# Kernel tuning notes

Hardware: AMD Instinct MI355X
Metric: run time of the kernel (lower is better)

Reference implementation:

```python
import jax, jax.numpy as jnp
import numpy as np
from jax import lax

# PSTConv constants (match init_kwargs)
R = 0.5            # ball-query radius
K = 32             # neighbors per anchor
SPATIAL_STRIDE = 2
TK = 3             # temporal kernel size (odd)
TSTRIDE = 1        # temporal stride
PAD = (1, 1)       # temporal padding, 'zeros' mode
MID = 128
OUT = 256


def setup_inputs() -> dict:
    key = jax.random.key(0)
    k1, k2, k3, k4, k5 = jax.random.split(key, 5)
    B, L, N, C = 8, 6, 2048, 64
    xyzs = jax.random.uniform(k1, (B, L, N, 3), dtype=jnp.float32)
    features = jax.random.normal(k2, (B, L, C, N), dtype=jnp.float32)
    # kaiming_uniform with size=[mid, in+3, 1, 1]: bound = 1/sqrt(in_planes+3)
    b = 1.0 / np.sqrt(C + 3)
    w_d = jax.random.uniform(k3, (MID, 3), minval=-b, maxval=b, dtype=jnp.float32)
    w_f = jax.random.uniform(k4, (MID, C), minval=-b, maxval=b, dtype=jnp.float32)
    bt = 1.0 / np.sqrt(TK * MID)
    w_t = jax.random.uniform(k5, (OUT, TK * MID), minval=-bt, maxval=bt, dtype=jnp.float32)
    return {"xyzs": xyzs, "features": features, "w_d": w_d, "w_f": w_f, "w_t": w_t}


def _fps(xyz, m):
    # furthest point sampling on [N,3]; CUDA kernel starts from index 0
    N = xyz.shape[0]
    def step(carry, _):
        dists, far = carry
        d = jnp.sum((xyz - xyz[far]) ** 2, axis=-1)
        dists = jnp.minimum(dists, d)
        nxt = jnp.argmax(dists).astype(jnp.int32)
        return (dists, nxt), far
    init = (jnp.full((N,), 1e10, dtype=xyz.dtype), jnp.int32(0))
    _, idx = lax.scan(step, init, None, length=m)
    return idx  # [m] int32


def _ball_query(nbr_xyz, anchor_xyz):
    # nbr_xyz [B,N,3], anchor_xyz [B,M,3] -> [B,M,K] int32 indices into N
    # Semantics of pointnet2 ball_query: first K points (in index order) within
    # radius R; slots past the count are filled with the first found index
    # (0 if no point is in range).
    N = nbr_xyz.shape[1]
    d2 = jnp.sum((anchor_xyz[:, :, None, :] - nbr_xyz[:, None, :, :]) ** 2, axis=-1)  # [B,M,N]
    vals = jnp.where(d2 < R * R, jnp.arange(N, dtype=jnp.int32), jnp.int32(N))
    neg_top, _ = lax.top_k(-vals, K)          # K smallest indices, ascending
    idx = -neg_top                            # [B,M,K]
    first = idx[..., :1]
    fill = jnp.where(first < N, first, 0)
    return jnp.where(idx < N, idx, fill)


def _group(feat, idx):
    # feat [B,C,N], idx [B,M,K] -> [B,C,M,K]
    return jax.vmap(lambda f, i: f[:, i])(feat, idx)


def reference(xyzs, features, w_d, w_f, w_t):
    B, L, N, _ = xyzs.shape
    M = N // SPATIAL_STRIDE
    rad = TK // 2
    # zero temporal padding
    zx = jnp.zeros((B, 1, N, 3), xyzs.dtype)
    zf = jnp.zeros((B, 1, features.shape[2], N), features.dtype)
    xp = jnp.concatenate([zx] * PAD[0] + [xyzs] + [zx] * PAD[1], axis=1)
    fp = jnp.concatenate([zf] * PAD[0] + [features] + [zf] * PAD[1], axis=1)
    Lp = L + PAD[0] + PAD[1]

    new_xyzs, new_feats = [], []
    fps_b = jax.vmap(lambda x: _fps(x, M))
    for t in range(rad, Lp - rad, TSTRIDE):
        xyz_t = xp[:, t]                                   # [B,N,3]
        aidx = fps_b(xyz_t)                                # [B,M]
        anchor = jnp.take_along_axis(xyz_t, aidx[:, :, None], axis=1)  # [B,M,3]
        anchor_c = jnp.transpose(anchor, (0, 2, 1))[:, :, :, None]     # [B,3,M,1]
        sfs = []
        for i in range(t - rad, t + rad + 1):
            idx = _ball_query(xp[:, i], anchor)            # [B,M,K]
            g_xyz = _group(jnp.transpose(xp[:, i], (0, 2, 1)), idx)    # [B,3,M,K]
            disp = g_xyz - anchor_c
            d = jnp.einsum('oc,bcmk->bomk', w_d, disp)     # [B,MID,M,K]
            g_f = _group(fp[:, i], idx)                    # [B,C,M,K]
            f = jnp.einsum('oc,bcmk->bomk', w_f, g_f)
            sfs.append(jnp.max(f + d, axis=-1))            # [B,MID,M]
        sf = jax.nn.relu(jnp.concatenate(sfs, axis=1))     # [B,TK*MID,M]
        new_feats.append(jnp.einsum('oc,bcm->bom', w_t, sf))
        new_xyzs.append(anchor)
    return jnp.stack(new_xyzs, axis=1), jnp.stack(new_feats, axis=1)
```

## Files before the change

### kernel.cpp

```cpp
#include <hip/hip_runtime.h>

#define BATCH 8
#define LFRM  6
#define NP    2048
#define MP    1024
#define CIN   64
#define MIDC  128
#define OUTC  256
#define TKM   384
#define KNN   32
#define RAD2  0.25f

#define FPS_BLOCKS (BATCH * LFRM)
#define WT_BLOCKS  ((OUTC * TKM) / (256 * 4))
#define FT_BLOCKS  (BATCH * LFRM * (NP / 64))
#define WFS 132

typedef float f2 __attribute__((ext_vector_type(2)));
typedef float f32x4 __attribute__((ext_vector_type(4)));
typedef _Float16 f16x8 __attribute__((ext_vector_type(8)));
typedef _Float16 f16x4 __attribute__((ext_vector_type(4)));

union SharedU {
  struct {
    float4 pts[NP];
    unsigned long long wk[2][4];
  } fps;
  struct {
    float ftile[CIN][64];
    float wfT[CIN][WFS];
    float xt[64], yt[64], zt[64];
    float wdl[MIDC * 3];
  } ft;
};

__device__ __forceinline__ uint64_t kmax64(uint64_t a, uint64_t b) {
  return a > b ? a : b;
}
template <int CTRL>
__device__ __forceinline__ uint64_t key_dpp(uint64_t k) {
  int lo = __builtin_amdgcn_update_dpp((int)(uint32_t)k, (int)(uint32_t)k,
                                       CTRL, 0xF, 0xF, false);
  int hi = __builtin_amdgcn_update_dpp((int)(uint32_t)(k >> 32),
                                       (int)(uint32_t)(k >> 32),
                                       CTRL, 0xF, 0xF, false);
  return ((uint64_t)(uint32_t)hi << 32) | (uint32_t)lo;
}

__device__ __forceinline__ f16x4 h4max(f16x4 a, f16x4 b) {
  f16x4 r;
  r[0] = a[0] > b[0] ? a[0] : b[0];
  r[1] = a[1] > b[1] ? a[1] : b[1];
  r[2] = a[2] > b[2] ? a[2] : b[2];
  r[3] = a[3] > b[3] ? a[3] : b[3];
  return r;
}

__device__ __forceinline__ void fps_path(const float* __restrict__ xyzs,
                                         float* __restrict__ out_xyz,
                                         SharedU* sh) {
#pragma clang fp contract(off)
  const int bt = blockIdx.x;
  const int tid = threadIdx.x;
  const int lane = tid & 63, wv = tid >> 6;
  const float* src = xyzs + (size_t)bt * NP * 3;

  for (int q = tid; q < NP; q += 256)
    sh->fps.pts[q] = make_float4(src[q * 3 + 0], src[q * 3 + 1], src[q * 3 + 2], 0.f);
  __syncthreads();

  f2 px[4], py[4], pz[4], dist[4];
#pragma unroll
  for (int u = 0; u < 4; ++u) {
    float4 a = sh->fps.pts[(wv * 8 + 2 * u) * 64 + lane];
    float4 b = sh->fps.pts[(wv * 8 + 2 * u + 1) * 64 + lane];
    px[u] = f2{a.x, b.x};
    py[u] = f2{a.y, b.y};
    pz[u] = f2{a.z, b.z};
    dist[u] = f2{1e10f, 1e10f};
  }

  float4 p0 = sh->fps.pts[0];
  float fx = p0.x, fy = p0.y, fz = p0.z;
  float* dst = out_xyz + (size_t)bt * MP * 3;

  for (int it = 0; it < MP; ++it) {
    if (tid == 0) {
      dst[it * 3 + 0] = fx;
      dst[it * 3 + 1] = fy;
      dst[it * 3 + 2] = fz;
    }
    const f2 fx2 = {fx, fx}, fy2 = {fy, fy}, fz2 = {fz, fz};
    float bv = -1.0f;
    int bsu = 0;
#pragma unroll
    for (int u = 0; u < 4; ++u) {
      f2 dx = px[u] - fx2;
      f2 dy = py[u] - fy2;
      f2 dz = pz[u] - fz2;
      f2 m = dx * dx;
      m = m + dy * dy;
      m = m + dz * dz;
      f2 nd = __builtin_elementwise_min(dist[u], m);
      dist[u] = nd;
      bool cx = nd.x > bv;
      bv = cx ? nd.x : bv;
      bsu = cx ? 2 * u : bsu;
      bool cy = nd.y > bv;
      bv = cy ? nd.y : bv;
      bsu = cy ? 2 * u + 1 : bsu;
    }
    const uint32_t p = (uint32_t)(((wv * 8 + bsu) << 6) | lane);
    uint64_t key = ((uint64_t)__float_as_uint(bv) << 32) | (uint32_t)(~p);
    key = kmax64(key, key_dpp<0x121>(key));
    key = kmax64(key, key_dpp<0x122>(key));
    key = kmax64(key, key_dpp<0x124>(key));
    key = kmax64(key, key_dpp<0x128>(key));
    key = kmax64(key, key_dpp<0x142>(key));
    key = kmax64(key, key_dpp<0x143>(key));

    const int par = it & 1;
    if (lane == 63) sh->fps.wk[par][wv] = key;
    __syncthreads();
    uint64_t k0 = kmax64(sh->fps.wk[par][0], sh->fps.wk[par][1]);
    uint64_t k1 = kmax64(sh->fps.wk[par][2], sh->fps.wk[par][3]);
    uint64_t kg = kmax64(k0, k1);
    const uint32_t wp = ~(uint32_t)kg;
    float4 w = sh->fps.pts[wp];
    fx = w.x; fy = w.y; fz = w.z;
  }
}

__device__ __forceinline__ void wt_path(const float* __restrict__ w_t,
                                        _Float16* __restrict__ wtH) {
  const int blk = blockIdx.x - FPS_BLOCKS;
  const int idx = (blk * 256 + (int)threadIdx.x) * 4;
  const float4 v = *(const float4*)&w_t[idx];
  f16x4 h;
  h[0] = (_Float16)v.x; h[1] = (_Float16)v.y;
  h[2] = (_Float16)v.z; h[3] = (_Float16)v.w;
  *(f16x4*)&wtH[idx] = h;
}

__device__ __forceinline__ void ftrans_path(const float* __restrict__ features,
                                            const float* __restrict__ w_f,
                                            const float* __restrict__ w_d,
                                            const float* __restrict__ xyzs,
                                            _Float16* __restrict__ G,
                                            SharedU* sh) {
  const int blk = blockIdx.x - FPS_BLOCKS - WT_BLOCKS;
  const int ntile = blk & 31;
  const int bl = blk >> 5;
  const int tid = threadIdx.x;

  const float* fsrc = features + (size_t)bl * CIN * NP + (size_t)ntile * 64;
  for (int idx = tid; idx < CIN * 64; idx += 256) {
    int c = idx >> 6, n = idx & 63;
    sh->ft.ftile[c][n] = fsrc[(size_t)c * NP + n];
  }
  for (int idx = tid; idx < CIN * MIDC; idx += 256) {
    int c = idx & 63, o = idx >> 6;
    sh->ft.wfT[c][o] = w_f[o * CIN + c];
  }
  if (tid < 64) {
    const float* xs = xyzs + ((size_t)bl * NP + (size_t)ntile * 64 + tid) * 3;
    sh->ft.xt[tid] = xs[0];
    sh->ft.yt[tid] = xs[1];
    sh->ft.zt[tid] = xs[2];
  }
  for (int idx = tid; idx < MIDC * 3; idx += 256) sh->ft.wdl[idx] = w_d[idx];
  __syncthreads();

  const int op = tid & 31;
  const int ng = tid >> 5;
  const int ob = op * 4;
  const int nb = ng * 8;

  float acc[4][8];
#pragma unroll
  for (int oo = 0; oo < 4; ++oo) {
    const float w0 = sh->ft.wdl[(ob + oo) * 3 + 0];
    const float w1 = sh->ft.wdl[(ob + oo) * 3 + 1];
    const float w2 = sh->ft.wdl[(ob + oo) * 3 + 2];
#pragma unroll
    for (int j = 0; j < 8; ++j)
      acc[oo][j] = w0 * sh->ft.xt[nb + j] + w1 * sh->ft.yt[nb + j] +
                   w2 * sh->ft.zt[nb + j];
  }

#pragma unroll 4
  for (int c = 0; c < CIN; ++c) {
    const float4 wq = *(const float4*)&sh->ft.wfT[c][ob];
    const float4 fA = *(const float4*)&sh->ft.ftile[c][nb];
    const float4 fB = *(const float4*)&sh->ft.ftile[c][nb + 4];
    const float wo[4] = {wq.x, wq.y, wq.z, wq.w};
    const float fv[8] = {fA.x, fA.y, fA.z, fA.w, fB.x, fB.y, fB.z, fB.w};
#pragma unroll
    for (int oo = 0; oo < 4; ++oo)
#pragma unroll
      for (int j = 0; j < 8; ++j)
        acc[oo][j] += wo[oo] * fv[j];
  }

  _Float16* dstp = G + ((size_t)bl * NP + (size_t)ntile * 64) * MIDC;
#pragma unroll
  for (int j = 0; j < 8; ++j) {
    f16x4 v;
    v[0] = (_Float16)acc[0][j]; v[1] = (_Float16)acc[1][j];
    v[2] = (_Float16)acc[2][j]; v[3] = (_Float16)acc[3][j];
    *(f16x4*)&dstp[(size_t)(nb + j) * MIDC + ob] = v;
  }
}

__global__ __launch_bounds__(256, 1) void fps_ftrans_kernel(
    const float* __restrict__ xyzs, const float* __restrict__ features,
    const float* __restrict__ w_f, const float* __restrict__ w_d,
    const float* __restrict__ w_t, float* __restrict__ out_xyz,
    _Float16* __restrict__ G, _Float16* __restrict__ wtH) {
  __shared__ SharedU sh;
  if (blockIdx.x < FPS_BLOCKS) {
    fps_path(xyzs, out_xyz, &sh);
    return;
  }
  if (blockIdx.x < FPS_BLOCKS + WT_BLOCKS) {
    wt_path(w_t, wtH);
    return;
  }
  ftrans_path(features, w_f, w_d, xyzs, G, &sh);
}

#define PSTR 392

__global__ __launch_bounds__(256) void pst_main(const float* __restrict__ xyzs,
                                                const float* __restrict__ w_d,
                                                const _Float16* __restrict__ wtH,
                                                const _Float16* __restrict__ G,
                                                const float* __restrict__ anchors,
                                                float* __restrict__ out_feat) {
  __shared__ union {
    float pxyz[NP * 3];
    _Float16 sf[32][PSTR];
  } u;
  __shared__ unsigned short nidx[32][KNN];
  __shared__ float anc[32][3];

  const int blk = (int)(blockIdx.x & 7) * 192 + (int)(blockIdx.x >> 3);
  const int mt = blk & 31;
  const int bt = blk >> 5;
  const int b = bt / LFRM;
  const int t = bt % LFRM + 1;
  const int tid = threadIdx.x;

  const float* asrc = anchors + ((size_t)bt * MP + (size_t)mt * 32) * 3;
  if (tid < 96) anc[tid / 3][tid % 3] = asrc[tid];
  __syncthreads();

  const int al = tid >> 3;
  const int j = tid & 7;
  const float ax = anc[al][0], ay = anc[al][1], az = anc[al][2];

  f16x4 wdah[4];
#pragma unroll
  for (int c4 = 0; c4 < 4; ++c4)
#pragma unroll
    for (int r = 0; r < 4; ++r) {
      int o = c4 * 32 + j * 4 + r;
      wdah[c4][r] = (_Float16)(w_d[o * 3 + 0] * ax + w_d[o * 3 + 1] * ay +
                               w_d[o * 3 + 2] * az);
    }
  const f16x4 hz = {(_Float16)0.f, (_Float16)0.f, (_Float16)0.f, (_Float16)0.f};

  const int lane = tid & 63, wv = tid >> 6;

  f16x4 hreg[3][4];

#pragma unroll
  for (int ii = 0; ii < 3; ++ii) {
    const int i = t - 1 + ii;

    if (i == 0 || i == LFRM + 1) {
#pragma unroll
      for (int c4 = 0; c4 < 4; ++c4)
        hreg[ii][c4] = h4max(hz - wdah[c4], hz);
    } else {
      const int f2i = i - 1;
      const float* fxyz = xyzs + (size_t)(b * LFRM + f2i) * NP * 3;
      __syncthreads();
      for (int q = tid; q < NP * 3; q += 256) u.pxyz[q] = fxyz[q];
      __syncthreads();

      for (int aa = 0; aa < 8; ++aa) {
        const int a = wv * 8 + aa;
        const float qx = anc[a][0], qy = anc[a][1], qz = anc[a][2];
        int total = 0;
        int fillidx = 0;
        for (int ch = 0; ch < NP / 64; ++ch) {
          const int p = ch * 64 + lane;
          float d2;
          {
#pragma clang fp contract(off)
            float dx = qx - u.pxyz[p * 3 + 0];
            float dy = qy - u.pxyz[p * 3 + 1];
            float dz = qz - u.pxyz[p * 3 + 2];
            d2 = dx * dx + dy * dy + dz * dz;
          }
          const bool inb = d2 < RAD2;
          const unsigned long long mk = __ballot(inb);
          if (mk != 0ull && total == 0)
            fillidx = ch * 64 + (int)__builtin_ctzll(mk);
          const int before = (int)__builtin_popcountll(mk & ((1ull << lane) - 1ull));
          const int slot = total + before;
          if (inb && slot < KNN) nidx[a][slot] = (unsigned short)p;
          total += (int)__builtin_popcountll(mk);
          if (total >= KNN) break;
        }
        const int nf = total < KNN ? total : KNN;
        if (lane < KNN - nf) nidx[a][nf + lane] = (unsigned short)fillidx;
      }

      const _Float16* gfr = G + (size_t)(b * LFRM + f2i) * NP * MIDC;
      f16x4 mh0 = {(_Float16)-6e4f, (_Float16)-6e4f, (_Float16)-6e4f, (_Float16)-6e4f};
      f16x4 mh1 = mh0, mh2 = mh0, mh3 = mh0;
#pragma unroll 4
      for (int k = 0; k < KNN; ++k) {
        const int p = nidx[al][k];
        const f16x4* row = (const f16x4*)(gfr + (size_t)p * MIDC);
        f16x4 v0 = row[j], v1 = row[8 + j], v2 = row[16 + j], v3 = row[24 + j];
        mh0 = h4max(mh0, v0);
        mh1 = h4max(mh1, v1);
        mh2 = h4max(mh2, v2);
        mh3 = h4max(mh3, v3);
      }
      hreg[ii][0] = h4max(mh0 - wdah[0], hz);
      hreg[ii][1] = h4max(mh1 - wdah[1], hz);
      hreg[ii][2] = h4max(mh2 - wdah[2], hz);
      hreg[ii][3] = h4max(mh3 - wdah[3], hz);
    }
  }

  __syncthreads();
#pragma unroll
  for (int ii = 0; ii < 3; ++ii)
#pragma unroll
    for (int c4 = 0; c4 < 4; ++c4)
      *(f16x4*)&u.sf[al][ii * MIDC + c4 * 32 + j * 4] = hreg[ii][c4];
  __syncthreads();

  const int l16 = lane & 15, lq = lane >> 4;
  f32x4 accm[4][2];
#pragma unroll
  for (int q = 0; q < 4; ++q)
#pragma unroll
    for (int n2 = 0; n2 < 2; ++n2) accm[q][n2] = f32x4{0.f, 0.f, 0.f, 0.f};

  for (int kc = 0; kc < TKM / 32; ++kc) {
    f16x8 bfr[2];
#pragma unroll
    for (int n2 = 0; n2 < 2; ++n2)
      bfr[n2] = *(const f16x8*)&u.sf[n2 * 16 + l16][kc * 32 + lq * 8];
#pragma unroll
    for (int q = 0; q < 4; ++q) {
      const int row = (wv * 4 + q) * 16 + l16;
      const f16x8 afr = *(const f16x8*)&wtH[(size_t)row * TKM + kc * 32 + lq * 8];
      accm[q][0] = __builtin_amdgcn_mfma_f32_16x16x32_f16(afr, bfr[0], accm[q][0], 0, 0, 0);
      accm[q][1] = __builtin_amdgcn_mfma_f32_16x16x32_f16(afr, bfr[1], accm[q][1], 0, 0, 0);
    }
  }

  float* ob = out_feat + (size_t)bt * OUTC * MP + (size_t)mt * 32;
#pragma unroll
  for (int q = 0; q < 4; ++q) {
    const int orow = (wv * 4 + q) * 16 + lq * 4;
#pragma unroll
    for (int n2 = 0; n2 < 2; ++n2)
#pragma unroll
      for (int r = 0; r < 4; ++r)
        ob[(size_t)(orow + r) * MP + n2 * 16 + l16] = accm[q][n2][r];
  }
}

extern "C" void kernel_launch(void* const* d_in, const int* in_sizes, int n_in,
                              void* d_out, int out_size, void* d_ws, size_t ws_size,
                              hipStream_t stream) {
  const float* xyzs = (const float*)d_in[0];
  const float* features = (const float*)d_in[1];
  const float* w_d = (const float*)d_in[2];
  const float* w_f = (const float*)d_in[3];
  const float* w_t = (const float*)d_in[4];

  float* out = (float*)d_out;
  float* out_xyz = out;
  float* out_feat = out + (size_t)BATCH * LFRM * MP * 3;
  _Float16* G = (_Float16*)d_ws;
  _Float16* wtH = G + (size_t)BATCH * LFRM * NP * MIDC;

  hipLaunchKernelGGL(fps_ftrans_kernel,
                     dim3(FPS_BLOCKS + WT_BLOCKS + FT_BLOCKS), dim3(256),
                     0, stream, xyzs, features, w_f, w_d, w_t, out_xyz, G, wtH);
  hipLaunchKernelGGL(pst_main, dim3(BATCH * LFRM * (MP / 32)), dim3(256), 0,
                     stream, xyzs, w_d, wtH, G, out_xyz, out_feat);
}
```

Baseline: 569.8 us.

## Process two FPS point clouds per block to interleave independent reductions

Each FPS block now handles two (batch, frame) clouds at once, halving the FPS block count. The two independent distance-update and DPP argmax chains are interleaved, and a single barrier per iteration serves both clouds. The intent is to hide the latency of the serial FPS loop, which is dominated by DPP reduction and barrier latency, by giving each wave more independent work. In exchange, LDS use doubles to about 64KB (which may limit occupancy or the union size), register pressure rises, and there are fewer blocks in flight.

After: 965.9 us. 1.7x slower.

```diff
diff --git a/kernel.cpp b/kernel.cpp
--- a/kernel.cpp
+++ b/kernel.cpp
@@ -11,7 +11,7 @@
 #define KNN   32
 #define RAD2  0.25f
 
-#define FPS_BLOCKS (BATCH * LFRM)
+#define FPS_BLOCKS ((BATCH * LFRM) / 2)
 #define WT_BLOCKS  ((OUTC * TKM) / (256 * 4))
 #define FT_BLOCKS  (BATCH * LFRM * (NP / 64))
 #define WFS 132
@@ -23,8 +23,10 @@
 
 union SharedU {
   struct {
-    float4 pts[NP];
-    unsigned long long wk[2][4];
+    float4 ptsA[NP];
+    float4 ptsB[NP];
+    unsigned long long wkA[2][4];
+    unsigned long long wkB[2][4];
   } fps;
   struct {
     float ftile[CIN][64];
@@ -60,74 +62,126 @@
                                          float* __restrict__ out_xyz,
                                          SharedU* sh) {
 #pragma clang fp contract(off)
-  const int bt = blockIdx.x;
+  const int bt0 = blockIdx.x * 2;
   const int tid = threadIdx.x;
   const int lane = tid & 63, wv = tid >> 6;
-  const float* src = xyzs + (size_t)bt * NP * 3;
-
-  for (int q = tid; q < NP; q += 256)
-    sh->fps.pts[q] = make_float4(src[q * 3 + 0], src[q * 3 + 1], src[q * 3 + 2], 0.f);
+  const float* srcA = xyzs + (size_t)bt0 * NP * 3;
+  const float* srcB = srcA + (size_t)NP * 3;
+
+  for (int q = tid; q < NP; q += 256) {
+    sh->fps.ptsA[q] = make_float4(srcA[q * 3 + 0], srcA[q * 3 + 1], srcA[q * 3 + 2], 0.f);
+    sh->fps.ptsB[q] = make_float4(srcB[q * 3 + 0], srcB[q * 3 + 1], srcB[q * 3 + 2], 0.f);
+  }
   __syncthreads();
 
-  f2 px[4], py[4], pz[4], dist[4];
+  f2 pxA[4], pyA[4], pzA[4], dA[4];
+  f2 pxB[4], pyB[4], pzB[4], dB[4];
 #pragma unroll
   for (int u = 0; u < 4; ++u) {
-    float4 a = sh->fps.pts[(wv * 8 + 2 * u) * 64 + lane];
-    float4 b = sh->fps.pts[(wv * 8 + 2 * u + 1) * 64 + lane];
-    px[u] = f2{a.x, b.x};
-    py[u] = f2{a.y, b.y};
-    pz[u] = f2{a.z, b.z};
-    dist[u] = f2{1e10f, 1e10f};
-  }
-
-  float4 p0 = sh->fps.pts[0];
-  float fx = p0.x, fy = p0.y, fz = p0.z;
-  float* dst = out_xyz + (size_t)bt * MP * 3;
+    float4 a0 = sh->fps.ptsA[(wv * 8 + 2 * u) * 64 + lane];
+    float4 a1 = sh->fps.ptsA[(wv * 8 + 2 * u + 1) * 64 + lane];
+    pxA[u] = f2{a0.x, a1.x}; pyA[u] = f2{a0.y, a1.y}; pzA[u] = f2{a0.z, a1.z};
+    dA[u] = f2{1e10f, 1e10f};
+    float4 b0 = sh->fps.ptsB[(wv * 8 + 2 * u) * 64 + lane];
+    float4 b1 = sh->fps.ptsB[(wv * 8 + 2 * u + 1) * 64 + lane];
+    pxB[u] = f2{b0.x, b1.x}; pyB[u] = f2{b0.y, b1.y}; pzB[u] = f2{b0.z, b1.z};
+    dB[u] = f2{1e10f, 1e10f};
+  }
+
+  float4 p0A = sh->fps.ptsA[0];
+  float4 p0B = sh->fps.ptsB[0];
+  float fxA = p0A.x, fyA = p0A.y, fzA = p0A.z;
+  float fxB = p0B.x, fyB = p0B.y, fzB = p0B.z;
+  float* dstA = out_xyz + (size_t)bt0 * MP * 3;
+  float* dstB = dstA + (size_t)MP * 3;
 
   for (int it = 0; it < MP; ++it) {
     if (tid == 0) {
-      dst[it * 3 + 0] = fx;
-      dst[it * 3 + 1] = fy;
-      dst[it * 3 + 2] = fz;
-    }
-    const f2 fx2 = {fx, fx}, fy2 = {fy, fy}, fz2 = {fz, fz};
-    float bv = -1.0f;
-    int bsu = 0;
-#pragma unroll
-    for (int u = 0; u < 4; ++u) {
-      f2 dx = px[u] - fx2;
-      f2 dy = py[u] - fy2;
-      f2 dz = pz[u] - fz2;
-      f2 m = dx * dx;
-      m = m + dy * dy;
-      m = m + dz * dz;
-      f2 nd = __builtin_elementwise_min(dist[u], m);
-      dist[u] = nd;
-      bool cx = nd.x > bv;
-      bv = cx ? nd.x : bv;
-      bsu = cx ? 2 * u : bsu;
-      bool cy = nd.y > bv;
-      bv = cy ? nd.y : bv;
-      bsu = cy ? 2 * u + 1 : bsu;
-    }
-    const uint32_t p = (uint32_t)(((wv * 8 + bsu) << 6) | lane);
-    uint64_t key = ((uint64_t)__float_as_uint(bv) << 32) | (uint32_t)(~p);
-    key = kmax64(key, key_dpp<0x121>(key));
-    key = kmax64(key, key_dpp<0x122>(key));
-    key = kmax64(key, key_dpp<0x124>(key));
-    key = kmax64(key, key_dpp<0x128>(key));
-    key = kmax64(key, key_dpp<0x142>(key));
-    key = kmax64(key, key_dpp<0x143>(key));
-
+      dstA[it * 3 + 0] = fxA; dstA[it * 3 + 1] = fyA; dstA[it * 3 + 2] = fzA;
+      dstB[it * 3 + 0] = fxB; dstB[it * 3 + 1] = fyB; dstB[it * 3 + 2] = fzB;
+    }
     const int par = it & 1;
-    if (lane == 63) sh->fps.wk[par][wv] = key;
+
+    {
+      const f2 fx2 = {fxA, fxA}, fy2 = {fyA, fyA}, fz2 = {fzA, fzA};
+      float bv = -1.0f;
+      int bsu = 0;
+#pragma unroll
+      for (int u = 0; u < 4; ++u) {
+        f2 dx = pxA[u] - fx2;
+        f2 dy = pyA[u] - fy2;
+        f2 dz = pzA[u] - fz2;
+        f2 m = dx * dx;
+        m = m + dy * dy;
+        m = m + dz * dz;
+        f2 nd = __builtin_elementwise_min(dA[u], m);
+        dA[u] = nd;
+        bool cx = nd.x > bv;
+        bv = cx ? nd.x : bv;
+        bsu = cx ? 2 * u : bsu;
+        bool cy = nd.y > bv;
+        bv = cy ? nd.y : bv;
+        bsu = cy ? 2 * u + 1 : bsu;
+      }
+      const uint32_t p = (uint32_t)(((wv * 8 + bsu) << 6) | lane);
+      uint64_t key = ((uint64_t)__float_as_uint(bv) << 32) | (uint32_t)(~p);
+      key = kmax64(key, key_dpp<0x121>(key));
+      key = kmax64(key, key_dpp<0x122>(key));
+      key = kmax64(key, key_dpp<0x124>(key));
+      key = kmax64(key, key_dpp<0x128>(key));
+      key = kmax64(key, key_dpp<0x142>(key));
+      key = kmax64(key, key_dpp<0x143>(key));
+      if (lane == 63) sh->fps.wkA[par][wv] = key;
+    }
+
+    {
+      const f2 fx2 = {fxB, fxB}, fy2 = {fyB, fyB}, fz2 = {fzB, fzB};
+      float bv = -1.0f;
+      int bsu = 0;
+#pragma unroll
+      for (int u = 0; u < 4; ++u) {
+        f2 dx = pxB[u] - fx2;
+        f2 dy = pyB[u] - fy2;
+        f2 dz = pzB[u] - fz2;
+        f2 m = dx * dx;
+        m = m + dy * dy;
+        m = m + dz * dz;
+        f2 nd = __builtin_elementwise_min(dB[u], m);
+        dB[u] = nd;
+        bool cx = nd.x > bv;
+        bv = cx ? nd.x : bv;
+        bsu = cx ? 2 * u : bsu;
+        bool cy = nd.y > bv;
+        bv = cy ? nd.y : bv;
+        bsu = cy ? 2 * u + 1 : bsu;
+      }
+      const uint32_t p = (uint32_t)(((wv * 8 + bsu) << 6) | lane);
+      uint64_t key = ((uint64_t)__float_as_uint(bv) << 32) | (uint32_t)(~p);
+      key = kmax64(key, key_dpp<0x121>(key));
+      key = kmax64(key, key_dpp<0x122>(key));
+      key = kmax64(key, key_dpp<0x124>(key));
+      key = kmax64(key, key_dpp<0x128>(key));
+      key = kmax64(key, key_dpp<0x142>(key));
+      key = kmax64(key, key_dpp<0x143>(key));
+      if (lane == 63) sh->fps.wkB[par][wv] = key;
+    }
+
     __syncthreads();
-    uint64_t k0 = kmax64(sh->fps.wk[par][0], sh->fps.wk[par][1]);
-    uint64_t k1 = kmax64(sh->fps.wk[par][2], sh->fps.wk[par][3]);
-    uint64_t kg = kmax64(k0, k1);
-    const uint32_t wp = ~(uint32_t)kg;
-    float4 w = sh->fps.pts[wp];
-    fx = w.x; fy = w.y; fz = w.z;
+
+    {
+      uint64_t k0 = kmax64(sh->fps.wkA[par][0], sh->fps.wkA[par][1]);
+      uint64_t k1 = kmax64(sh->fps.wkA[par][2], sh->fps.wkA[par][3]);
+      const uint32_t wp = ~(uint32_t)kmax64(k0, k1);
+      float4 w = sh->fps.ptsA[wp];
+      fxA = w.x; fyA = w.y; fzA = w.z;
+    }
+    {
+      uint64_t k0 = kmax64(sh->fps.wkB[par][0], sh->fps.wkB[par][1]);
+      uint64_t k1 = kmax64(sh->fps.wkB[par][2], sh->fps.wkB[par][3]);
+      const uint32_t wp = ~(uint32_t)kmax64(k0, k1);
+      float4 w = sh->fps.ptsB[wp];
+      fxB = w.x; fyB = w.y; fzB = w.z;
+    }
   }
 }
 
```
